# Kernel tuning notes

Hardware: AMD Instinct MI355X
Metric: run time of the kernel (lower is better)

The kernel has to match this reference:

```python
import jax, jax.numpy as jnp
import numpy as np

MIN_NORM = 1e-15
PROJ_EPS = 4e-3  # hgcn PoincareBall eps for float32
C = 1.0          # curvature (constant across both layers)


def _norm(x):
    return jnp.clip(jnp.linalg.norm(x, axis=-1, keepdims=True), MIN_NORM)


def _artanh(x):
    return jnp.arctanh(jnp.clip(x, -1.0 + 1e-7, 1.0 - 1e-7))


def proj(x, c):
    # clip points inside the Poincare ball of curvature c
    n = _norm(x)
    maxnorm = (1.0 - PROJ_EPS) / jnp.sqrt(c)
    return jnp.where(n > maxnorm, x / n * maxnorm, x)


def expmap0(u, c):
    sc = jnp.sqrt(c)
    n = _norm(u)
    return jnp.tanh(sc * n) * u / (sc * n)


def logmap0(p, c):
    sc = jnp.sqrt(c)
    n = _norm(p)
    return _artanh(sc * n) * p / (sc * n)


def mobius_add(x, y, c):
    x2 = jnp.sum(x * x, -1, keepdims=True)
    y2 = jnp.sum(y * y, -1, keepdims=True)
    xy = jnp.sum(x * y, -1, keepdims=True)
    num = (1.0 + 2.0 * c * xy + c * y2) * x + (1.0 - c * x2) * y
    den = 1.0 + 2.0 * c * xy + (c ** 2) * x2 * y2
    return num / jnp.clip(den, MIN_NORM)


def mobius_matvec(W, x, c):
    sc = jnp.sqrt(c)
    xn = _norm(x)
    mx = x @ W.T
    mxn = _norm(mx)
    res = jnp.tanh(mxn / xn * _artanh(sc * xn)) * mx / (mxn * sc)
    zero = jnp.all(mx == 0, axis=-1, keepdims=True)
    return jnp.where(zero, jnp.zeros((), x.dtype), res)


def hgc_layer(x, W, b, src, dst, ew, c_in, c_out, N):
    # HypLinear: mobius matvec + hyperbolic bias
    h = proj(mobius_matvec(W, x, c_in), c_in)
    hyp_b = proj(expmap0(b[None, :], c_in), c_in)  # proj_tan0 is identity
    h = proj(mobius_add(h, hyp_b, c_in), c_in)
    # HypAgg: tangent-space sparse aggregation
    xt = logmap0(h, c_in)                               # [N, d]
    msg = ew[:, None] * xt[src]                          # [E, d] gather
    agg = jax.ops.segment_sum(msg, dst, num_segments=N)  # spmm(adj, xt)
    h = proj(expmap0(agg, c_in), c_in)
    # HypAct: relu in tangent space, remap with c_out
    xt = jax.nn.relu(logmap0(h, c_in))
    return proj(expmap0(xt, c_out), c_out)


def setup_inputs() -> dict:
    key = jax.random.key(0)
    ks = jax.random.split(key, 8)
    N, F, H, D, E = 100000, 128, 128, 128, 1600000
    s = 1.0 / np.sqrt(F)
    x = jax.random.normal(ks[0], (N, F), jnp.float32) * 0.1
    W1 = jax.random.normal(ks[1], (H, F), jnp.float32) * s
    b1 = jax.random.normal(ks[2], (H,), jnp.float32) * 0.01
    W2 = jax.random.normal(ks[3], (D, H), jnp.float32) * s
    b2 = jax.random.normal(ks[4], (D,), jnp.float32) * 0.01
    edge_weight = jax.random.uniform(ks[5], (E,), jnp.float32) * (1.0 / 16.0)
    src = jax.random.randint(ks[6], (E,), 0, N)
    dst = jax.random.randint(ks[7], (E,), 0, N)
    return {"x": x, "W1": W1, "b1": b1, "W2": W2, "b2": b2,
            "edge_weight": edge_weight, "src": src, "dst": dst}


def reference(x, W1, b1, W2, b2, edge_weight, src, dst):
    N = x.shape[0]
    # HGCN.encode: map Euclidean features onto the manifold
    xh = proj(expmap0(x, C), C)  # proj_tan0 is identity for PoincareBall
    h = hgc_layer(xh, W1, b1, src, dst, edge_weight, C, C, N)
    h = hgc_layer(h, W2, b2, src, dst, edge_weight, C, C, N)
    return h
```

## Files before the change

kernel.cpp:

```cpp
#include <hip/hip_runtime.h>
#include <hip/hip_bf16.h>

#define MINN 1e-15f
#define MAXN (1.0f - 4e-3f)
#define ATMAX 3.1063031f

#define NBH 9
#define BNODES 512
#define BCAP 10240
#define BWIN (BCAP + 4 * BNODES)
#define PBE 8192

typedef short short8 __attribute__((ext_vector_type(8)));
typedef float f32x4 __attribute__((ext_vector_type(4)));

__device__ __forceinline__ float wsum(float v) {
    v += __shfl_xor(v, 32, 64);
    v += __shfl_xor(v, 16, 64);
    v += __shfl_xor(v, 8, 64);
    v += __shfl_xor(v, 4, 64);
    v += __shfl_xor(v, 2, 64);
    v += __shfl_xor(v, 1, 64);
    return v;
}

__device__ __forceinline__ void splitf(float f, short& hi, short& lo) {
    unsigned u = __float_as_uint(f);
    hi = (short)(u >> 16);
    float r = f - __uint_as_float(u & 0xffff0000u);
    lo = (short)(__float_as_uint(r) >> 16);
}

__device__ __forceinline__ unsigned pack_bf16(float a, float b) {
    unsigned ua = __float_as_uint(a);
    unsigned ub = __float_as_uint(b);
    ua = (ua + 0x7fffu + ((ua >> 16) & 1u)) >> 16;
    ub = (ub + 0x7fffu + ((ub >> 16) & 1u)) & 0xffff0000u;
    return ua | ub;
}

__global__ __launch_bounds__(256) void k_bucket(const int* __restrict__ src, const int* __restrict__ dst,
                                                const float* __restrict__ ew, int* __restrict__ gcur,
                                                int2* __restrict__ staging, int E, int NBUCK) {
    __shared__ int hist[512];
    const int tid = threadIdx.x;
    const int e0 = blockIdx.x * PBE;
    for (int i = tid; i < 512; i += 256) hist[i] = 0;
    __syncthreads();
    #pragma unroll 4
    for (int j = 0; j < PBE / 256; j++) {
        int e = e0 + j * 256 + tid;
        if (e < E) atomicAdd(&hist[dst[e] >> NBH], 1);
    }
    __syncthreads();
    for (int b = tid; b < NBUCK; b += 256) {
        int c = hist[b];
        hist[b] = c ? atomicAdd(&gcur[b], c) : 0;
    }
    __syncthreads();
    #pragma unroll 4
    for (int j = 0; j < PBE / 256; j++) {
        int e = e0 + j * 256 + tid;
        if (e < E) {
            int d = dst[e];
            int bkt = d >> NBH;
            int pos = atomicAdd(&hist[bkt], 1);
            if (pos < BCAP)
                staging[(size_t)bkt * BCAP + pos] =
                    make_int2((src[e] & 0x1FFFF) | ((d & (BNODES - 1)) << 17), __float_as_int(ew[e]));
        }
    }
}

__global__ __launch_bounds__(256) void k_cbuild(const int* __restrict__ gcur, const int2* __restrict__ staging,
                                                int2* __restrict__ csr, int2* __restrict__ rp2, int N) {
    __shared__ int cnt[BNODES];
    __shared__ int base[BNODES];
    __shared__ int sbuf[256];
    const int tid = threadIdx.x;
    const int b = blockIdx.x;
    const int bcnt = min(gcur[b], BCAP);
    const int wbase = b * BWIN;
    const int2* st = staging + (size_t)b * BCAP;

    for (int i = tid; i < BNODES; i += 256) cnt[i] = 0;
    __syncthreads();
    for (int i = tid; i < bcnt; i += 256) {
        int nl = (st[i].x >> 17) & (BNODES - 1);
        atomicAdd(&cnt[nl], 1);
    }
    __syncthreads();
    int p0 = (cnt[2 * tid] + 3) & ~3;
    int p1 = (cnt[2 * tid + 1] + 3) & ~3;
    int s = p0 + p1;
    sbuf[tid] = s;
    __syncthreads();
    for (int off = 1; off < 256; off <<= 1) {
        int add = (tid >= off) ? sbuf[tid - off] : 0;
        __syncthreads();
        sbuf[tid] += add;
        __syncthreads();
    }
    int excl = sbuf[tid] - s;
    base[2 * tid] = excl;
    base[2 * tid + 1] = excl + p0;
    __syncthreads();
    for (int i = tid; i < BNODES; i += 256) {
        int node = b * BNODES + i;
        int c = cnt[i];
        int pd = (c + 3) & ~3;
        int gb = wbase + base[i];
        if (node < N) rp2[node] = make_int2(gb, pd);
        for (int k = c; k < pd; k++) csr[gb + k] = make_int2(0, 0);
    }
    __syncthreads();
    for (int i = tid; i < BNODES; i += 256) cnt[i] = wbase + base[i];
    __syncthreads();
    for (int i = tid; i < bcnt; i += 256) {
        int2 p = st[i];
        int nl = (p.x >> 17) & (BNODES - 1);
        int pos = atomicAdd(&cnt[nl], 1);
        csr[pos] = make_int2(p.x & 0x1FFFF, p.y);
    }
}

__global__ __launch_bounds__(256) void k_linear(
    const float* __restrict__ X, const float* __restrict__ W, const float* __restrict__ B,
    const float2* __restrict__ NRM, unsigned* __restrict__ OUT, int N, int do_encode)
{
    __shared__ float mxs[16][132];
    __shared__ float xn2s[16];

    const int lane = threadIdx.x & 63;
    const int wid = threadIdx.x >> 6;
    const int lr = lane & 15;
    const int lg = lane >> 4;

    short8 Bh[2][4], Bl[2][4];
    #pragma unroll
    for (int ct = 0; ct < 2; ct++) {
        const float* wr = W + (wid * 32 + ct * 16 + lr) * 128 + lg * 8;
        #pragma unroll
        for (int kt = 0; kt < 4; kt++) {
            float4 w0 = *(const float4*)(wr + kt * 32);
            float4 w1 = *(const float4*)(wr + kt * 32 + 4);
            float wv[8] = {w0.x, w0.y, w0.z, w0.w, w1.x, w1.y, w1.z, w1.w};
            #pragma unroll
            for (int i = 0; i < 8; i++) {
                short h, l; splitf(wv[i], h, l);
                Bh[ct][kt][i] = h; Bl[ct][kt][i] = l;
            }
        }
    }

    float2 bb = *(const float2*)(B + 2 * lane);
    float nb2 = wsum(bb.x * bb.x + bb.y * bb.y);
    float nb = fmaxf(sqrtf(nb2), MINN);
    float tbc = fminf(tanhf(nb), MAXN);
    float fb = tbc / nb;
    float hb0 = fb * bb.x, hb1 = fb * bb.y;
    float y2 = tbc * tbc;

    const int ntiles = (N + 15) >> 4;
    for (int t = blockIdx.x; t < ntiles; t += gridDim.x) {
        const int row0 = t << 4;
        const int arow = row0 + lr;
        const bool rv = arow < N;

        short8 Ah[4], Al[4];
        float xn2 = 0.f;
        const float* xr = X + (size_t)arow * 128 + lg * 8;
        #pragma unroll
        for (int kt = 0; kt < 4; kt++) {
            float4 a0 = rv ? *(const float4*)(xr + kt * 32) : make_float4(0.f, 0.f, 0.f, 0.f);
            float4 a1 = rv ? *(const float4*)(xr + kt * 32 + 4) : make_float4(0.f, 0.f, 0.f, 0.f);
            float av[8] = {a0.x, a0.y, a0.z, a0.w, a1.x, a1.y, a1.z, a1.w};
            #pragma unroll
            for (int i = 0; i < 8; i++) {
                xn2 = fmaf(av[i], av[i], xn2);
                short h, l; splitf(av[i], h, l);
                Ah[kt][i] = h; Al[kt][i] = l;
            }
        }
        xn2 += __shfl_xor(xn2, 16, 64);
        xn2 += __shfl_xor(xn2, 32, 64);

        f32x4 acc0 = {0.f, 0.f, 0.f, 0.f}, acc1 = {0.f, 0.f, 0.f, 0.f};
        #pragma unroll
        for (int kt = 0; kt < 4; kt++) {
            acc0 = __builtin_amdgcn_mfma_f32_16x16x32_bf16(Ah[kt], Bh[0][kt], acc0, 0, 0, 0);
            acc1 = __builtin_amdgcn_mfma_f32_16x16x32_bf16(Ah[kt], Bh[1][kt], acc1, 0, 0, 0);
            acc0 = __builtin_amdgcn_mfma_f32_16x16x32_bf16(Al[kt], Bh[0][kt], acc0, 0, 0, 0);
            acc1 = __builtin_amdgcn_mfma_f32_16x16x32_bf16(Al[kt], Bh[1][kt], acc1, 0, 0, 0);
            acc0 = __builtin_amdgcn_mfma_f32_16x16x32_bf16(Ah[kt], Bl[0][kt], acc0, 0, 0, 0);
            acc1 = __builtin_amdgcn_mfma_f32_16x16x32_bf16(Ah[kt], Bl[1][kt], acc1, 0, 0, 0);
        }

        #pragma unroll
        for (int r = 0; r < 4; r++) {
            mxs[lg * 4 + r][wid * 32 + lr] = acc0[r];
            mxs[lg * 4 + r][wid * 32 + 16 + lr] = acc1[r];
        }
        if (wid == 0 && lane < 16) xn2s[lane] = xn2;
        __syncthreads();

        float mn2[4], dmb[4];
        float2 mvv[4];
        #pragma unroll
        for (int r = 0; r < 4; r++) {
            mvv[r] = *(const float2*)&mxs[wid * 4 + r][2 * lane];
            mn2[r] = mvv[r].x * mvv[r].x + mvv[r].y * mvv[r].y;
            dmb[r] = mvv[r].x * hb0 + mvv[r].y * hb1;
        }
        #pragma unroll
        for (int s = 32; s; s >>= 1) {
            #pragma unroll
            for (int r = 0; r < 4; r++) {
                mn2[r] += __shfl_xor(mn2[r], s, 64);
                dmb[r] += __shfl_xor(dmb[r], s, 64);
            }
        }
        #pragma unroll
        for (int r = 0; r < 4; r++) {
            const int lrow = wid * 4 + r;
            const int row = row0 + lrow;
            if (row < N) {
                float xn, axn;
                if (do_encode) {
                    float n0 = fmaxf(sqrtf(xn2s[lrow]), MINN);
                    xn = n0;
                    axn = fminf(n0, ATMAX);
                } else {
                    float2 nr = NRM[row];
                    xn = fmaxf(nr.x, MINN);
                    axn = nr.y;
                }
                float mxn = fmaxf(sqrtf(mn2[r]), MINN);
                float arg = (mxn / xn) * axn;
                float thc = fminf(tanhf(arg), MAXN);
                float f1 = thc / mxn;
                float x2 = thc * thc;
                float xy = f1 * dmb[r];
                float ca = 1.f + 2.f * xy + y2;
                float cb = 1.f - x2;
                float inv = 1.f / fmaxf(1.f + 2.f * xy + x2 * y2, MINN);
                float ng2 = inv * inv * (ca * ca * x2 + 2.f * ca * cb * xy + cb * cb * y2);
                float ng = fmaxf(sqrtf(ng2), MINN);
                float lf = atanhf(fminf(ng, MAXN)) / ng;
                float sle = lf * inv;
                float o0 = sle * (ca * f1 * mvv[r].x + cb * hb0);
                float o1 = sle * (ca * f1 * mvv[r].y + cb * hb1);
                OUT[(size_t)row * 64 + lane] = pack_bf16(o0, o1);
            }
        }
        __syncthreads();
    }
}

__global__ __launch_bounds__(256) void k_aggact(const unsigned* __restrict__ XT, const int2* __restrict__ rp2,
                                                const int2* __restrict__ csr,
                                                float* __restrict__ OUT, float2* __restrict__ NRM, int N) {
    const int lane = threadIdx.x & 63;
    const int wid = threadIdx.x >> 6;
    int node = blockIdx.x * 4 + wid;
    if (node >= N) return;
    int2 rr = rp2[node];
    int b = __builtin_amdgcn_readfirstlane(rr.x);
    int cnt = __builtin_amdgcn_readfirstlane(rr.y);
    int e8 = b + (cnt & ~7);

    float ax[8], ay[8];
    #pragma unroll
    for (int j = 0; j < 8; j++) { ax[j] = 0.f; ay[j] = 0.f; }

    for (int i = b; i < e8; i += 8) {
        int2 c[8];
        #pragma unroll
        for (int j = 0; j < 8; j++) c[j] = csr[i + j];
        unsigned v[8];
        #pragma unroll
        for (int j = 0; j < 8; j++) v[j] = XT[(size_t)c[j].x * 64 + lane];
        #pragma unroll
        for (int j = 0; j < 8; j++) {
            float w = __int_as_float(c[j].y);
            float f0 = __uint_as_float(v[j] << 16);
            float f1 = __uint_as_float(v[j] & 0xffff0000u);
            ax[j] = fmaf(w, f0, ax[j]);
            ay[j] = fmaf(w, f1, ay[j]);
        }
    }
    if (cnt & 4) {
        int i = e8;
        int2 c[4];
        #pragma unroll
        for (int j = 0; j < 4; j++) c[j] = csr[i + j];
        unsigned v[4];
        #pragma unroll
        for (int j = 0; j < 4; j++) v[j] = XT[(size_t)c[j].x * 64 + lane];
        #pragma unroll
        for (int j = 0; j < 4; j++) {
            float w = __int_as_float(c[j].y);
            float f0 = __uint_as_float(v[j] << 16);
            float f1 = __uint_as_float(v[j] & 0xffff0000u);
            ax[j] = fmaf(w, f0, ax[j]);
            ay[j] = fmaf(w, f1, ay[j]);
        }
    }
    float a0 = ((ax[0] + ax[1]) + (ax[2] + ax[3])) + ((ax[4] + ax[5]) + (ax[6] + ax[7]));
    float a1 = ((ay[0] + ay[1]) + (ay[2] + ay[3])) + ((ay[4] + ay[5]) + (ay[6] + ay[7]));

    float r0 = fmaxf(a0, 0.f), r1 = fmaxf(a1, 0.f);
    float n2 = a0 * a0 + a1 * a1;
    float q2 = r0 * r0 + r1 * r1;
    #pragma unroll
    for (int s = 32; s; s >>= 1) {
        n2 += __shfl_xor(n2, s, 64);
        q2 += __shfl_xor(q2, s, 64);
    }
    float n = fmaxf(sqrtf(n2), MINN);
    float cp = fminf(n, ATMAX) / n;
    float nq = fmaxf(cp * sqrtf(q2), MINN);
    float tq = fminf(tanhf(nq), MAXN);
    float f2 = tq / nq;
    float sc = f2 * cp;
    *(float2*)(OUT + (size_t)node * 128 + 2 * lane) = make_float2(sc * r0, sc * r1);
    if (lane == 0) NRM[node] = make_float2(tq, fminf(nq, ATMAX));
}

extern "C" void kernel_launch(void* const* d_in, const int* in_sizes, int n_in,
                              void* d_out, int out_size, void* d_ws, size_t ws_size,
                              hipStream_t stream) {
    const float* x  = (const float*)d_in[0];
    const float* W1 = (const float*)d_in[1];
    const float* b1 = (const float*)d_in[2];
    const float* W2 = (const float*)d_in[3];
    const float* b2 = (const float*)d_in[4];
    const float* ew = (const float*)d_in[5];
    const int* src  = (const int*)d_in[6];
    const int* dst  = (const int*)d_in[7];
    const int N = in_sizes[0] / 128;
    const int E = in_sizes[5];
    float* out = (float*)d_out;

    const int NBUCK = (N + BNODES - 1) >> NBH;
    const int EB = (E + PBE - 1) / PBE;

    char* w = (char*)d_ws;
    unsigned* xt = (unsigned*)w; w += (size_t)N * 64 * 4;
    int2*   csr  = (int2*)w;   w += (size_t)NBUCK * BWIN * 8;
    float2* nrm  = (float2*)w; w += (size_t)N * 8;
    int2*   rp2  = (int2*)w;   w += (size_t)N * 8;
    int2*   staging = (int2*)w; w += (size_t)NBUCK * BCAP * 8;
    int*    gcur = (int*)w;    w += (size_t)NBUCK * 4 + 256;

    hipMemsetAsync(gcur, 0, (size_t)NBUCK * 4, stream);
    k_bucket<<<EB, 256, 0, stream>>>(src, dst, ew, gcur, staging, E, NBUCK);
    k_cbuild<<<NBUCK, 256, 0, stream>>>(gcur, staging, csr, rp2, N);

    const int rowblocks = (N + 3) / 4;
    k_linear<<<1024, 256, 0, stream>>>(x, W1, b1, nrm, xt, N, 1);
    k_aggact<<<rowblocks, 256, 0, stream>>>(xt, rp2, csr, out, nrm, N);
    k_linear<<<1024, 256, 0, stream>>>(out, W2, b2, nrm, xt, N, 0);
    k_aggact<<<rowblocks, 256, 0, stream>>>(xt, rp2, csr, out, nrm, N);
}
```

Baseline: 344.7 us.

## Pre-split weights and activations into bf16 hi/lo buffers, one tile per block

Moves the fp32-to-bf16 hi/lo splitting of weights and bias preprocessing into small prep kernels, so k_linear no longer re-splits W or recomputes the bias in every block. The first-layer input is encoded by a new k_encode kernel, and the layer-1 aggregation now writes pre-split hi/lo activations instead of fp32. k_linear drops the persistent grid-stride loop and launches one 16-row tile per block. tanh and atanh are replaced with exp/log/rcp fast approximations. The changes add kernel launches and extra hi/lo buffer traffic, and the fast math may slightly alter accuracy.

New measurement: 358.7 us. 4.1% more time.

```diff
diff --git a/kernel.cpp b/kernel.cpp
--- a/kernel.cpp
+++ b/kernel.cpp
@@ -31,12 +31,24 @@
     lo = (short)(__float_as_uint(r) >> 16);
 }
 
+__device__ __forceinline__ unsigned packsplit_hi(short ha, short hb) {
+    return (unsigned)(unsigned short)ha | ((unsigned)(unsigned short)hb << 16);
+}
+
 __device__ __forceinline__ unsigned pack_bf16(float a, float b) {
     unsigned ua = __float_as_uint(a);
     unsigned ub = __float_as_uint(b);
     ua = (ua + 0x7fffu + ((ua >> 16) & 1u)) >> 16;
     ub = (ub + 0x7fffu + ((ub >> 16) & 1u)) & 0xffff0000u;
     return ua | ub;
+}
+
+__device__ __forceinline__ float tanh_fast(float x) {
+    float e = __expf(2.f * x);
+    return (e - 1.f) * __builtin_amdgcn_rcpf(e + 1.f);
+}
+__device__ __forceinline__ float atanh_fast(float x) {
+    return 0.5f * __logf((1.f + x) * __builtin_amdgcn_rcpf(1.f - x));
 }
 
 __global__ __launch_bounds__(256) void k_bucket(const int* __restrict__ src, const int* __restrict__ dst,
@@ -124,142 +136,159 @@
     }
 }
 
+__global__ __launch_bounds__(256) void k_wprep(const float* __restrict__ W1, const float* __restrict__ W2,
+                                               unsigned* __restrict__ WH1, unsigned* __restrict__ WL1,
+                                               unsigned* __restrict__ WH2, unsigned* __restrict__ WL2) {
+    int i = (blockIdx.x & 31) * 256 + threadIdx.x;
+    const float* W = (blockIdx.x < 32) ? W1 : W2;
+    unsigned* WH = (blockIdx.x < 32) ? WH1 : WH2;
+    unsigned* WL = (blockIdx.x < 32) ? WL1 : WL2;
+    float a = W[2 * i], b = W[2 * i + 1];
+    short ha, la, hb, lb;
+    splitf(a, ha, la); splitf(b, hb, lb);
+    WH[i] = packsplit_hi(ha, hb);
+    WL[i] = packsplit_hi(la, lb);
+}
+
+__global__ __launch_bounds__(64) void k_bias(const float* __restrict__ B1, const float* __restrict__ B2,
+                                             float2* __restrict__ HB) {
+    const int lane = threadIdx.x;
+    const float* B = (blockIdx.x == 0) ? B1 : B2;
+    float2 bb = *(const float2*)(B + 2 * lane);
+    float nb2 = wsum(bb.x * bb.x + bb.y * bb.y);
+    float nb = fmaxf(sqrtf(nb2), MINN);
+    float tbc = fminf(tanh_fast(nb), MAXN);
+    float fb = tbc / nb;
+    HB[blockIdx.x * 65 + lane] = make_float2(fb * bb.x, fb * bb.y);
+    if (lane == 0) HB[blockIdx.x * 65 + 64] = make_float2(tbc * tbc, 0.f);
+}
+
+__global__ __launch_bounds__(256) void k_encode(const float* __restrict__ X,
+                                                unsigned* __restrict__ XH, unsigned* __restrict__ XL,
+                                                float2* __restrict__ NRM, int N) {
+    const int lane = threadIdx.x & 63;
+    const int wid = threadIdx.x >> 6;
+    int row = blockIdx.x * 4 + wid;
+    if (row >= N) return;
+    float2 u = *(const float2*)(X + (size_t)row * 128 + 2 * lane);
+    float n2 = wsum(u.x * u.x + u.y * u.y);
+    short h0, l0, h1, l1;
+    splitf(u.x, h0, l0); splitf(u.y, h1, l1);
+    XH[(size_t)row * 64 + lane] = packsplit_hi(h0, h1);
+    XL[(size_t)row * 64 + lane] = packsplit_hi(l0, l1);
+    if (lane == 0) {
+        float n0 = fmaxf(sqrtf(n2), MINN);
+        NRM[row] = make_float2(n0, fminf(n0, ATMAX));
+    }
+}
+
 __global__ __launch_bounds__(256) void k_linear(
-    const float* __restrict__ X, const float* __restrict__ W, const float* __restrict__ B,
-    const float2* __restrict__ NRM, unsigned* __restrict__ OUT, int N, int do_encode)
+    const unsigned* __restrict__ XH, const unsigned* __restrict__ XL,
+    const unsigned* __restrict__ WH, const unsigned* __restrict__ WL,
+    const float2* __restrict__ HB, const float2* __restrict__ NRM,
+    unsigned* __restrict__ OUT, int N)
 {
     __shared__ float mxs[16][132];
-    __shared__ float xn2s[16];
 
     const int lane = threadIdx.x & 63;
     const int wid = threadIdx.x >> 6;
     const int lr = lane & 15;
     const int lg = lane >> 4;
+    const int row0 = blockIdx.x << 4;
 
     short8 Bh[2][4], Bl[2][4];
     #pragma unroll
     for (int ct = 0; ct < 2; ct++) {
-        const float* wr = W + (wid * 32 + ct * 16 + lr) * 128 + lg * 8;
+        const int nrow = wid * 32 + ct * 16 + lr;
         #pragma unroll
         for (int kt = 0; kt < 4; kt++) {
-            float4 w0 = *(const float4*)(wr + kt * 32);
-            float4 w1 = *(const float4*)(wr + kt * 32 + 4);
-            float wv[8] = {w0.x, w0.y, w0.z, w0.w, w1.x, w1.y, w1.z, w1.w};
-            #pragma unroll
-            for (int i = 0; i < 8; i++) {
-                short h, l; splitf(wv[i], h, l);
-                Bh[ct][kt][i] = h; Bl[ct][kt][i] = l;
-            }
-        }
-    }
-
-    float2 bb = *(const float2*)(B + 2 * lane);
-    float nb2 = wsum(bb.x * bb.x + bb.y * bb.y);
-    float nb = fmaxf(sqrtf(nb2), MINN);
-    float tbc = fminf(tanhf(nb), MAXN);
-    float fb = tbc / nb;
-    float hb0 = fb * bb.x, hb1 = fb * bb.y;
-    float y2 = tbc * tbc;
-
-    const int ntiles = (N + 15) >> 4;
-    for (int t = blockIdx.x; t < ntiles; t += gridDim.x) {
-        const int row0 = t << 4;
-        const int arow = row0 + lr;
-        const bool rv = arow < N;
-
-        short8 Ah[4], Al[4];
-        float xn2 = 0.f;
-        const float* xr = X + (size_t)arow * 128 + lg * 8;
-        #pragma unroll
-        for (int kt = 0; kt < 4; kt++) {
-            float4 a0 = rv ? *(const float4*)(xr + kt * 32) : make_float4(0.f, 0.f, 0.f, 0.f);
-            float4 a1 = rv ? *(const float4*)(xr + kt * 32 + 4) : make_float4(0.f, 0.f, 0.f, 0.f);
-            float av[8] = {a0.x, a0.y, a0.z, a0.w, a1.x, a1.y, a1.z, a1.w};
-            #pragma unroll
-            for (int i = 0; i < 8; i++) {
-                xn2 = fmaf(av[i], av[i], xn2);
-                short h, l; splitf(av[i], h, l);
-                Ah[kt][i] = h; Al[kt][i] = l;
-            }
-        }
-        xn2 += __shfl_xor(xn2, 16, 64);
-        xn2 += __shfl_xor(xn2, 32, 64);
-
-        f32x4 acc0 = {0.f, 0.f, 0.f, 0.f}, acc1 = {0.f, 0.f, 0.f, 0.f};
-        #pragma unroll
-        for (int kt = 0; kt < 4; kt++) {
-            acc0 = __builtin_amdgcn_mfma_f32_16x16x32_bf16(Ah[kt], Bh[0][kt], acc0, 0, 0, 0);
-            acc1 = __builtin_amdgcn_mfma_f32_16x16x32_bf16(Ah[kt], Bh[1][kt], acc1, 0, 0, 0);
-            acc0 = __builtin_amdgcn_mfma_f32_16x16x32_bf16(Al[kt], Bh[0][kt], acc0, 0, 0, 0);
-            acc1 = __builtin_amdgcn_mfma_f32_16x16x32_bf16(Al[kt], Bh[1][kt], acc1, 0, 0, 0);
-            acc0 = __builtin_amdgcn_mfma_f32_16x16x32_bf16(Ah[kt], Bl[0][kt], acc0, 0, 0, 0);
-            acc1 = __builtin_amdgcn_mfma_f32_16x16x32_bf16(Ah[kt], Bl[1][kt], acc1, 0, 0, 0);
-        }
-
+            Bh[ct][kt] = *(const short8*)(WH + nrow * 64 + kt * 16 + lg * 4);
+            Bl[ct][kt] = *(const short8*)(WL + nrow * 64 + kt * 16 + lg * 4);
+        }
+    }
+    float2 hb = HB[lane];
+    float y2 = HB[64].x;
+
+    const int arow = row0 + lr;
+    const bool rv = arow < N;
+    short8 Ah[4], Al[4];
+    #pragma unroll
+    for (int kt = 0; kt < 4; kt++) {
+        if (rv) {
+            Ah[kt] = *(const short8*)(XH + (size_t)arow * 64 + kt * 16 + lg * 4);
+            Al[kt] = *(const short8*)(XL + (size_t)arow * 64 + kt * 16 + lg * 4);
+        } else {
+            Ah[kt] = short8{0,0,0,0,0,0,0,0};
+            Al[kt] = short8{0,0,0,0,0,0,0,0};
+        }
+    }
+
+    f32x4 acc0 = {0.f, 0.f, 0.f, 0.f}, acc1 = {0.f, 0.f, 0.f, 0.f};
+    #pragma unroll
+    for (int kt = 0; kt < 4; kt++) {
+        acc0 = __builtin_amdgcn_mfma_f32_16x16x32_bf16(Ah[kt], Bh[0][kt], acc0, 0, 0, 0);
+        acc1 = __builtin_amdgcn_mfma_f32_16x16x32_bf16(Ah[kt], Bh[1][kt], acc1, 0, 0, 0);
+        acc0 = __builtin_amdgcn_mfma_f32_16x16x32_bf16(Al[kt], Bh[0][kt], acc0, 0, 0, 0);
+        acc1 = __builtin_amdgcn_mfma_f32_16x16x32_bf16(Al[kt], Bh[1][kt], acc1, 0, 0, 0);
+        acc0 = __builtin_amdgcn_mfma_f32_16x16x32_bf16(Ah[kt], Bl[0][kt], acc0, 0, 0, 0);
+        acc1 = __builtin_amdgcn_mfma_f32_16x16x32_bf16(Ah[kt], Bl[1][kt], acc1, 0, 0, 0);
+    }
+
+    #pragma unroll
+    for (int r = 0; r < 4; r++) {
+        mxs[lg * 4 + r][wid * 32 + lr] = acc0[r];
+        mxs[lg * 4 + r][wid * 32 + 16 + lr] = acc1[r];
+    }
+    __syncthreads();
+
+    float mn2[4], dmb[4];
+    float2 mvv[4];
+    #pragma unroll
+    for (int r = 0; r < 4; r++) {
+        mvv[r] = *(const float2*)&mxs[wid * 4 + r][2 * lane];
+        mn2[r] = mvv[r].x * mvv[r].x + mvv[r].y * mvv[r].y;
+        dmb[r] = mvv[r].x * hb.x + mvv[r].y * hb.y;
+    }
+    #pragma unroll
+    for (int s = 32; s; s >>= 1) {
         #pragma unroll
         for (int r = 0; r < 4; r++) {
-            mxs[lg * 4 + r][wid * 32 + lr] = acc0[r];
-            mxs[lg * 4 + r][wid * 32 + 16 + lr] = acc1[r];
-        }
-        if (wid == 0 && lane < 16) xn2s[lane] = xn2;
-        __syncthreads();
-
-        float mn2[4], dmb[4];
-        float2 mvv[4];
-        #pragma unroll
-        for (int r = 0; r < 4; r++) {
-            mvv[r] = *(const float2*)&mxs[wid * 4 + r][2 * lane];
-            mn2[r] = mvv[r].x * mvv[r].x + mvv[r].y * mvv[r].y;
-            dmb[r] = mvv[r].x * hb0 + mvv[r].y * hb1;
-        }
-        #pragma unroll
-        for (int s = 32; s; s >>= 1) {
-            #pragma unroll
-            for (int r = 0; r < 4; r++) {
-                mn2[r] += __shfl_xor(mn2[r], s, 64);
-                dmb[r] += __shfl_xor(dmb[r], s, 64);
-            }
-        }
-        #pragma unroll
-        for (int r = 0; r < 4; r++) {
-            const int lrow = wid * 4 + r;
-            const int row = row0 + lrow;
-            if (row < N) {
-                float xn, axn;
-                if (do_encode) {
-                    float n0 = fmaxf(sqrtf(xn2s[lrow]), MINN);
-                    xn = n0;
-                    axn = fminf(n0, ATMAX);
-                } else {
-                    float2 nr = NRM[row];
-                    xn = fmaxf(nr.x, MINN);
-                    axn = nr.y;
-                }
-                float mxn = fmaxf(sqrtf(mn2[r]), MINN);
-                float arg = (mxn / xn) * axn;
-                float thc = fminf(tanhf(arg), MAXN);
-                float f1 = thc / mxn;
-                float x2 = thc * thc;
-                float xy = f1 * dmb[r];
-                float ca = 1.f + 2.f * xy + y2;
-                float cb = 1.f - x2;
-                float inv = 1.f / fmaxf(1.f + 2.f * xy + x2 * y2, MINN);
-                float ng2 = inv * inv * (ca * ca * x2 + 2.f * ca * cb * xy + cb * cb * y2);
-                float ng = fmaxf(sqrtf(ng2), MINN);
-                float lf = atanhf(fminf(ng, MAXN)) / ng;
-                float sle = lf * inv;
-                float o0 = sle * (ca * f1 * mvv[r].x + cb * hb0);
-                float o1 = sle * (ca * f1 * mvv[r].y + cb * hb1);
-                OUT[(size_t)row * 64 + lane] = pack_bf16(o0, o1);
-            }
-        }
-        __syncthreads();
+            mn2[r] += __shfl_xor(mn2[r], s, 64);
+            dmb[r] += __shfl_xor(dmb[r], s, 64);
+        }
+    }
+    #pragma unroll
+    for (int r = 0; r < 4; r++) {
+        const int row = row0 + wid * 4 + r;
+        if (row < N) {
+            float2 nr = NRM[row];
+            float xn = fmaxf(nr.x, MINN);
+            float axn = nr.y;
+            float mxn = fmaxf(sqrtf(mn2[r]), MINN);
+            float arg = (mxn / xn) * axn;
+            float thc = fminf(tanh_fast(arg), MAXN);
+            float f1 = thc / mxn;
+            float x2 = thc * thc;
+            float xy = f1 * dmb[r];
+            float ca = 1.f + 2.f * xy + y2;
+            float cb = 1.f - x2;
+            float inv = 1.f / fmaxf(1.f + 2.f * xy + x2 * y2, MINN);
+            float ng2 = inv * inv * (ca * ca * x2 + 2.f * ca * cb * xy + cb * cb * y2);
+            float ng = fmaxf(sqrtf(ng2), MINN);
+            float lf = atanh_fast(fminf(ng, MAXN)) / ng;
+            float sle = lf * inv;
+            float o0 = sle * (ca * f1 * mvv[r].x + cb * hb.x);
+            float o1 = sle * (ca * f1 * mvv[r].y + cb * hb.y);
+            OUT[(size_t)row * 64 + lane] = pack_bf16(o0, o1);
+        }
     }
 }
 
 __global__ __launch_bounds__(256) void k_aggact(const unsigned* __restrict__ XT, const int2* __restrict__ rp2,
                                                 const int2* __restrict__ csr,
-                                                float* __restrict__ OUT, float2* __restrict__ NRM, int N) {
+                                                float* __restrict__ OUTF,
+                                                unsigned* __restrict__ OUTH, unsigned* __restrict__ OUTL,
+                                                float2* __restrict__ NRM, int N, int last) {
     const int lane = threadIdx.x & 63;
     const int wid = threadIdx.x >> 6;
     int node = blockIdx.x * 4 + wid;
@@ -283,10 +312,8 @@
         #pragma unroll
         for (int j = 0; j < 8; j++) {
             float w = __int_as_float(c[j].y);
-            float f0 = __uint_as_float(v[j] << 16);
-            float f1 = __uint_as_float(v[j] & 0xffff0000u);
-            ax[j] = fmaf(w, f0, ax[j]);
-            ay[j] = fmaf(w, f1, ay[j]);
+            ax[j] = fmaf(w, __uint_as_float(v[j] << 16), ax[j]);
+            ay[j] = fmaf(w, __uint_as_float(v[j] & 0xffff0000u), ay[j]);
         }
     }
     if (cnt & 4) {
@@ -300,10 +327,8 @@
         #pragma unroll
         for (int j = 0; j < 4; j++) {
             float w = __int_as_float(c[j].y);
-            float f0 = __uint_as_float(v[j] << 16);
-            float f1 = __uint_as_float(v[j] & 0xffff0000u);
-            ax[j] = fmaf(w, f0, ax[j]);
-            ay[j] = fmaf(w, f1, ay[j]);
+            ax[j] = fmaf(w, __uint_as_float(v[j] << 16), ax[j]);
+            ay[j] = fmaf(w, __uint_as_float(v[j] & 0xffff0000u), ay[j]);
         }
     }
     float a0 = ((ax[0] + ax[1]) + (ax[2] + ax[3])) + ((ax[4] + ax[5]) + (ax[6] + ax[7]));
@@ -320,11 +345,19 @@
     float n = fmaxf(sqrtf(n2), MINN);
     float cp = fminf(n, ATMAX) / n;
     float nq = fmaxf(cp * sqrtf(q2), MINN);
-    float tq = fminf(tanhf(nq), MAXN);
+    float tq = fminf(tanh_fast(nq), MAXN);
     float f2 = tq / nq;
     float sc = f2 * cp;
-    *(float2*)(OUT + (size_t)node * 128 + 2 * lane) = make_float2(sc * r0, sc * r1);
-    if (lane == 0) NRM[node] = make_float2(tq, fminf(nq, ATMAX));
+    float o0 = sc * r0, o1 = sc * r1;
+    if (last) {
+        *(float2*)(OUTF + (size_t)node * 128 + 2 * lane) = make_float2(o0, o1);
+    } else {
+        short h0, l0, h1, l1;
+        splitf(o0, h0, l0); splitf(o1, h1, l1);
+        OUTH[(size_t)node * 64 + lane] = packsplit_hi(h0, h1);
+        OUTL[(size_t)node * 64 + lane] = packsplit_hi(l0, l1);
+        if (lane == 0) NRM[node] = make_float2(tq, fminf(nq, ATMAX));
+    }
 }
 
 extern "C" void kernel_launch(void* const* d_in, const int* in_sizes, int n_in,
@@ -346,20 +379,33 @@
     const int EB = (E + PBE - 1) / PBE;
 
     char* w = (char*)d_ws;
-    unsigned* xt = (unsigned*)w; w += (size_t)N * 64 * 4;
-    int2*   csr  = (int2*)w;   w += (size_t)NBUCK * BWIN * 8;
-    float2* nrm  = (float2*)w; w += (size_t)N * 8;
-    int2*   rp2  = (int2*)w;   w += (size_t)N * 8;
+    unsigned* xt  = (unsigned*)w; w += (size_t)N * 64 * 4;
+    unsigned* xh  = (unsigned*)w; w += (size_t)N * 64 * 4;
+    unsigned* xl  = (unsigned*)w; w += (size_t)N * 64 * 4;
+    int2*   csr   = (int2*)w;   w += (size_t)NBUCK * BWIN * 8;
+    float2* nrmA  = (float2*)w; w += (size_t)N * 8;
+    float2* nrmB  = (float2*)w; w += (size_t)N * 8;
+    int2*   rp2   = (int2*)w;   w += (size_t)N * 8;
     int2*   staging = (int2*)w; w += (size_t)NBUCK * BCAP * 8;
-    int*    gcur = (int*)w;    w += (size_t)NBUCK * 4 + 256;
+    unsigned* wh1 = (unsigned*)w; w += 8192 * 4;
+    unsigned* wl1 = (unsigned*)w; w += 8192 * 4;
+    unsigned* wh2 = (unsigned*)w; w += 8192 * 4;
+    unsigned* wl2 = (unsigned*)w; w += 8192 * 4;
+    float2* hbuf  = (float2*)w; w += 2 * 65 * 8;
+    int*    gcur  = (int*)w;    w += (size_t)NBUCK * 4 + 256;
 
     hipMemsetAsync(gcur, 0, (size_t)NBUCK * 4, stream);
     k_bucket<<<EB, 256, 0, stream>>>(src, dst, ew, gcur, staging, E, NBUCK);
     k_cbuild<<<NBUCK, 256, 0, stream>>>(gcur, staging, csr, rp2, N);
+    k_wprep<<<64, 256, 0, stream>>>(W1, W2, wh1, wl1, wh2, wl2);
+    k_bias<<<2, 64, 0, stream>>>(b1, b2, hbuf);
 
     const int rowblocks = (N + 3) / 4;
-    k_linear<<<1024, 256, 0, stream>>>(x, W1, b1, nrm, xt, N, 1);
-    k_aggact<<<rowblocks, 256, 0, stream>>>(xt, rp2, csr, out, nrm, N);
-    k_linear<<<1024, 256, 0, stream>>>(out, W2, b2, nrm, xt, N, 0);
-    k_aggact<<<rowblocks, 256, 0, stream>>>(xt, rp2, csr, out, nrm, N);
-}
+    const int ntiles = (N + 15) / 16;
+
+    k_encode<<<rowblocks, 256, 0, stream>>>(x, xh, xl, nrmA, N);
+    k_linear<<<ntiles, 256, 0, stream>>>(xh, xl, wh1, wl1, hbuf, nrmA, xt, N);
+    k_aggact<<<rowblocks, 256, 0, stream>>>(xt, rp2, csr, nullptr, xh, xl, nrmB, N, 0);
+    k_linear<<<ntiles, 256, 0, stream>>>(xh, xl, wh2, wl2, hbuf + 65, nrmB, xt, N);
+    k_aggact<<<rowblocks, 256, 0, stream>>>(xt, rp2, csr, out, nullptr, nullptr, nullptr, N, 1);
+}
```
